# Performance work log

Measured on AMD Instinct MI355X. Metric: run time of the kernel, lower is better.

Reference implementation:

```python
import jax, jax.numpy as jnp
import numpy as np

B, S, H = 2, 1024, 2048          # batch, seq, hidden_size
I = 7168                          # intermediate_size
E = 8                             # num_local_experts
TOPK = 2                          # num_experts_per_tok
R = int(I * H * 0.1 / (I + H))    # delta_low_rank = 159


def setup_inputs() -> dict:
    key = jax.random.key(0)
    ks = jax.random.split(key, 12)
    s = 0.02
    return {
        "hidden_states": jax.random.normal(ks[0], (B, S, H), jnp.float32),
        "gate_w": jax.random.normal(ks[1], (E, H), jnp.float32) * s,
        "W1": jax.random.normal(ks[2], (E, I, H), jnp.float32) * s,
        "W2": jax.random.normal(ks[3], (E, H, I), jnp.float32) * s,
        "W3": jax.random.normal(ks[4], (E, I, H), jnp.float32) * s,
        "U1": jax.random.normal(ks[5], (E, I, R), jnp.float32) * s,
        "V1": jax.random.normal(ks[6], (E, R, H), jnp.float32) * s,
        "U2": jax.random.normal(ks[7], (E, H, R), jnp.float32) * s,
        "V2": jax.random.normal(ks[8], (E, R, I), jnp.float32) * s,
        "U3": jax.random.normal(ks[9], (E, I, R), jnp.float32) * s,
        "V3": jax.random.normal(ks[10], (E, R, H), jnp.float32) * s,
    }


def reference(hidden_states, gate_w, W1, W2, W3, U1, V1, U2, V2, U3, V3):
    b, s, h = hidden_states.shape
    x = hidden_states.reshape(-1, h)                     # [T, H]
    T = x.shape[0]
    router_logits = x @ gate_w.T                          # [T, E]
    probs = jax.nn.softmax(router_logits.astype(jnp.float32), axis=-1)
    rw, sel = jax.lax.top_k(probs, TOPK)                  # [T, k]
    rw = rw / jnp.sum(rw, axis=-1, keepdims=True)
    rw = rw.astype(x.dtype)
    # dense combine weights: zero for unselected experts (same math as gather/scatter)
    comb = jnp.zeros((T, E), x.dtype).at[jnp.arange(T)[:, None], sel].add(rw)
    out = jnp.zeros_like(x)
    for e in range(E):                                    # small fixed expert loop
        up = x @ W3[e].T + (x @ V3[e].T) @ U3[e].T        # [T, I]
        gate = x @ W1[e].T + (x @ V1[e].T) @ U1[e].T      # [T, I]
        hmid = jax.nn.silu(gate) * up                     # [T, I]
        y = hmid @ W2[e].T + (hmid @ V2[e].T) @ U2[e].T   # [T, H]
        out = out + comb[:, e, None] * y
    return out.reshape(b, s, h), router_logits
```

## Files before the change

kernel.cpp:

```cpp
#include <hip/hip_runtime.h>
#include <cstdint>
#include <cstddef>

#define TT 2048
#define HH 2048
#define II 7168
#define EE 8
#define RR 159
#define RPAD 192
#define ROWS 4096

typedef __attribute__((ext_vector_type(8))) short bf16x8;
typedef __attribute__((ext_vector_type(4))) float f32x4;

__device__ __forceinline__ unsigned short f2bf(float f) {
  unsigned int u = __float_as_uint(f);
  u += 0x7fffu + ((u >> 16) & 1u);
  return (unsigned short)(u >> 16);
}
__device__ __forceinline__ bf16x8 zero8() {
  bf16x8 v;
#pragma unroll
  for (int j = 0; j < 8; j++) v[j] = 0;
  return v;
}
__device__ __forceinline__ void gload16(const unsigned short* g, unsigned short* l) {
  __builtin_amdgcn_global_load_lds(
      (const __attribute__((address_space(1))) unsigned int*)g,
      (__attribute__((address_space(3))) unsigned int*)l, 16, 0, 0);
}

__global__ __launch_bounds__(256) void k_f2bf_flat(const float* __restrict__ s,
                                                   unsigned short* __restrict__ d,
                                                   long long n8) {
  long long i = (long long)blockIdx.x * blockDim.x + threadIdx.x;
  long long stride = (long long)gridDim.x * blockDim.x;
  for (; i < n8; i += stride) {
    const float* p = s + i * 8;
    float4 a = *(const float4*)p;
    float4 b = *(const float4*)(p + 4);
    bf16x8 v;
    v[0] = (short)f2bf(a.x); v[1] = (short)f2bf(a.y);
    v[2] = (short)f2bf(a.z); v[3] = (short)f2bf(a.w);
    v[4] = (short)f2bf(b.x); v[5] = (short)f2bf(b.y);
    v[6] = (short)f2bf(b.z); v[7] = (short)f2bf(b.w);
    *(bf16x8*)(d + i * 8) = v;
  }
}

__global__ __launch_bounds__(256) void k_upad(const float* __restrict__ U,
                                              unsigned short* __restrict__ Up, int rows) {
  long long idx = (long long)blockIdx.x * 256 + threadIdx.x;
  long long total = (long long)rows * 24;
  if (idx >= total) return;
  int row = (int)(idx / 24), c8 = (int)(idx % 24);
  unsigned short* dp = Up + (size_t)row * RPAD + c8 * 8;
#pragma unroll
  for (int j = 0; j < 8; j++) {
    int c = c8 * 8 + j;
    dp[j] = (c < RR) ? f2bf(U[(size_t)row * RR + c]) : (unsigned short)0;
  }
}

__global__ __launch_bounds__(256) void k_router(
    const float* __restrict__ x, const float* __restrict__ gw,
    float* __restrict__ logits_out, int* __restrict__ sel,
    float* __restrict__ wtok, int* __restrict__ counts) {
  int t = blockIdx.x;
  const float* xr = x + (size_t)t * HH;
  int base = threadIdx.x * 8;
  float4 x0 = *(const float4*)(xr + base);
  float4 x1 = *(const float4*)(xr + base + 4);
  float part[EE];
#pragma unroll
  for (int e = 0; e < EE; e++) {
    const float* g = gw + (size_t)e * HH + base;
    float4 g0 = *(const float4*)g;
    float4 g1 = *(const float4*)(g + 4);
    part[e] = x0.x * g0.x + x0.y * g0.y + x0.z * g0.z + x0.w * g0.w +
              x1.x * g1.x + x1.y * g1.y + x1.z * g1.z + x1.w * g1.w;
  }
#pragma unroll
  for (int off = 32; off > 0; off >>= 1)
#pragma unroll
    for (int e = 0; e < EE; e++) part[e] += __shfl_down(part[e], off);
  __shared__ float red[4][EE];
  int w = threadIdx.x >> 6, lane = threadIdx.x & 63;
  if (lane == 0) {
#pragma unroll
    for (int e = 0; e < EE; e++) red[w][e] = part[e];
  }
  __syncthreads();
  if (threadIdx.x == 0) {
    float lg[EE];
    float mx = -1e30f;
#pragma unroll
    for (int e = 0; e < EE; e++) {
      lg[e] = red[0][e] + red[1][e] + red[2][e] + red[3][e];
      logits_out[(size_t)t * EE + e] = lg[e];
      mx = fmaxf(mx, lg[e]);
    }
// ... 79 lines not shown
  float* Pout = Pp + (size_t)blockIdx.z * ROWS * RPAD;
  int kt0 = split * kc;
  int kt1 = kt0 + kc;
  if (kt1 > K) kt1 = K;
  __shared__ unsigned short As[64 * 64];
  __shared__ unsigned short Bs[192 * 64];
  int tid = threadIdx.x, lane = tid & 63, w = tid >> 6;
  int rstage = tid >> 3, cg = tid & 7;
  f32x4 acc[12];
#pragma unroll
  for (int n = 0; n < 12; n++) acc[n] = (f32x4){0.f, 0.f, 0.f, 0.f};
  for (int kt = kt0; kt < kt1; kt += 64) {
#pragma unroll
    for (int p = 0; p < 2; p++) {
      int r = p * 32 + rstage;
      bf16x8 v = zero8();
      int gr = m0 + r;
      if (gr < cnt) {
        size_t arow = GATHER ? (size_t)rowsA[roff + gr] : (size_t)(roff + gr);
        v = *(const bf16x8*)(Ab + arow * (size_t)lda + kt + cg * 8);
      }
      *(bf16x8*)&As[r * 64 + ((cg ^ (r & 7)) * 8)] = v;
    }
#pragma unroll
    for (int p = 0; p < 6; p++) {
      int r = p * 32 + rstage;
      bf16x8 v = zero8();
      if (r < RR) v = *(const bf16x8*)(V + (size_t)r * K + kt + cg * 8);
      *(bf16x8*)&Bs[r * 64 + ((cg ^ (r & 7)) * 8)] = v;
    }
    __syncthreads();
#pragma unroll
    for (int ks = 0; ks < 2; ks++) {
      int rA = w * 16 + (lane & 15);
      bf16x8 a = *(const bf16x8*)&As[rA * 64 + (((ks * 4 + (lane >> 4)) ^ (rA & 7)) * 8)];
#pragma unroll
      for (int n = 0; n < 12; n++) {
        int rB = n * 16 + (lane & 15);
        bf16x8 b = *(const bf16x8*)&Bs[rB * 64 + (((ks * 4 + (lane >> 4)) ^ (rB & 7)) * 8)];
        acc[n] = __builtin_amdgcn_mfma_f32_16x16x32_bf16(a, b, acc[n], 0, 0, 0);
      }
    }
    __syncthreads();
  }
  int mbase = m0 + w * 16 + (lane >> 4) * 4;
#pragma unroll
  for (int n = 0; n < 12; n++) {
    int col = n * 16 + (lane & 15);
#pragma unroll
    for (int r4 = 0; r4 < 4; r4++) {
      int row = mbase + r4;
      if (row < cnt) Pout[(size_t)(roff + row) * RPAD + col] = acc[n][r4];
    }
  }
}

__global__ __launch_bounds__(256) void k_lr_reduce(
    const float* __restrict__ Pp, unsigned short* __restrict__ P0,
    unsigned short* __restrict__ P1m, int NS, int nmat) {
  long long idx = (long long)blockIdx.x * 256 + threadIdx.x;
  long long total = (long long)nmat * ROWS * 24;
  if (idx >= total) return;
  int mat = (int)(idx / ((long long)ROWS * 24));
  int rem = (int)(idx % ((long long)ROWS * 24));
  int row = rem / 24, c8 = rem % 24;
  const float* base = Pp + ((size_t)mat * NS) * ROWS * RPAD + (size_t)row * RPAD + c8 * 8;
  float s0 = 0, s1 = 0, s2 = 0, s3 = 0, s4 = 0, s5 = 0, s6 = 0, s7 = 0;
  for (int sp = 0; sp < NS; sp++) {
    const float* p = base + (size_t)sp * ROWS * RPAD;
    float4 a = *(const float4*)p;
    float4 b = *(const float4*)(p + 4);
    s0 += a.x; s1 += a.y; s2 += a.z; s3 += a.w;
    s4 += b.x; s5 += b.y; s6 += b.z; s7 += b.w;
  }
  bf16x8 v;
  v[0] = (short)f2bf(s0); v[1] = (short)f2bf(s1);
  v[2] = (short)f2bf(s2); v[3] = (short)f2bf(s3);
  v[4] = (short)f2bf(s4); v[5] = (short)f2bf(s5);
  v[6] = (short)f2bf(s6); v[7] = (short)f2bf(s7);
  unsigned short* P = (mat == 0) ? P0 : P1m;
  *(bf16x8*)(P + (size_t)row * RPAD + c8 * 8) = v;
}

template <bool GATHER>
__global__ __launch_bounds__(256, 2) void k_lowrank(
    const unsigned short* __restrict__ Ab, int lda, int K,
    const float* __restrict__ Vaf, const float* __restrict__ Vbf,
    unsigned short* __restrict__ Pa, unsigned short* __restrict__ Pb,
    const int* __restrict__ counts, const int* __restrict__ offs,
    const int* __restrict__ rowsA) {
  int e = blockIdx.y;
  int cnt = counts[e];
  int m0 = blockIdx.x * 64;
  if (m0 >= cnt) return;
  int roff = offs[e];
  unsigned short* P = (blockIdx.z == 0) ? Pa : Pb;
  __shared__ unsigned short As[64 * 64];
  __shared__ unsigned short Bs[192 * 64];
  int tid = threadIdx.x, lane = tid & 63, w = tid >> 6;
  int rstage = tid >> 3, cg = tid & 7;
  f32x4 acc[12];
#pragma unroll
  for (int n = 0; n < 12; n++) acc[n] = (f32x4){0.f, 0.f, 0.f, 0.f};
  for (int kt = 0; kt < K; kt += 64) {
#pragma unroll
    for (int p = 0; p < 2; p++) {
      int r = p * 32 + rstage;
      bf16x8 v = zero8();
      int gr = m0 + r;
      if (gr < cnt) {
        size_t arow = GATHER ? (size_t)rowsA[roff + gr] : (size_t)(roff + gr);
        v = *(const bf16x8*)(Ab + arow * (size_t)lda + kt + cg * 8);
      }
      *(bf16x8*)&As[r * 64 + ((cg ^ (r & 7)) * 8)] = v;
    }
#pragma unroll
    for (int p = 0; p < 6; p++) {
      int r = p * 32 + rstage;
      bf16x8 v = zero8();
      if (r < RR) {
        const float* V = ((blockIdx.z == 0) ? Vaf : Vbf) + (size_t)e * RR * K;
        const float* s = V + (size_t)r * K + kt + cg * 8;
        float4 a = *(const float4*)s;
        float4 b = *(const float4*)(s + 4);
        v[0] = (short)f2bf(a.x); v[1] = (short)f2bf(a.y);
        v[2] = (short)f2bf(a.z); v[3] = (short)f2bf(a.w);
        v[4] = (short)f2bf(b.x); v[5] = (short)f2bf(b.y);
        v[6] = (short)f2bf(b.z); v[7] = (short)f2bf(b.w);
      }
      *(bf16x8*)&Bs[r * 64 + ((cg ^ (r & 7)) * 8)] = v;
    }
    __syncthreads();
#pragma unroll
    for (int ks = 0; ks < 2; ks++) {
      int rA = w * 16 + (lane & 15);
      bf16x8 a = *(const bf16x8*)&As[rA * 64 + (((ks * 4 + (lane >> 4)) ^ (rA & 7)) * 8)];
#pragma unroll
      for (int n = 0; n < 12; n++) {
        int rB = n * 16 + (lane & 15);
        bf16x8 b = *(const bf16x8*)&Bs[rB * 64 + (((ks * 4 + (lane >> 4)) ^ (rB & 7)) * 8)];
        acc[n] = __builtin_amdgcn_mfma_f32_16x16x32_bf16(a, b, acc[n], 0, 0, 0);
      }
    }
    __syncthreads();
  }
  int mbase = m0 + w * 16 + (lane >> 4) * 4;
#pragma unroll
  for (int n = 0; n < 12; n++) {
    int col = n * 16 + (lane & 15);
#pragma unroll
    for (int r4 = 0; r4 < 4; r4++) {
      int row = mbase + r4;
      if (row < cnt) P[(size_t)(roff + row) * RPAD + col] = f2bf(acc[n][r4]);
    }
  }
}

template <bool PRE>
__global__ __launch_bounds__(256, 2) void k_mlp1(
    const unsigned short* __restrict__ Xb,
    const float* __restrict__ W1f, const float* __restrict__ W3f,
    const unsigned short* __restrict__ W1b, const unsigned short* __restrict__ W3b,
    const unsigned short* __restrict__ P1, const unsigned short* __restrict__ P3,
    const float* __restrict__ U1f, const float* __restrict__ U3f,
    const unsigned short* __restrict__ U1p, const unsigned short* __restrict__ U3p,
    unsigned short* __restrict__ hmid,
    const int* __restrict__ counts, const int* __restrict__ offs,
    const int* __restrict__ rowsA) {
  int e = blockIdx.z;
  int cnt = counts[e];
  int m0 = blockIdx.y * 128;
  if (m0 >= cnt) return;
  int n0 = blockIdx.x * 128;
  int roff = offs[e];
  __shared__ unsigned short As[128 * 64];
  __shared__ unsigned short Bg[128 * 64];
  __shared__ unsigned short Bu[128 * 64];
  int tid = threadIdx.x, lane = tid & 63, w = tid >> 6;
  int wr = (w >> 1) * 64, wc = (w & 1) * 64;
  int rstage = tid >> 3, cg = tid & 7;
  f32x4 accg[4][4], accu[4][4];
#pragma unroll
  for (int m = 0; m < 4; m++)
#pragma unroll
    for (int n = 0; n < 4; n++) {
      accg[m][n] = (f32x4){0.f, 0.f, 0.f, 0.f};
      accu[m][n] = (f32x4){0.f, 0.f, 0.f, 0.f};
    }
  int srow = (w << 5) + (lane >> 3);
  int swz = (((lane & 7) ^ ((lane >> 3) & 7)) << 3);
  const unsigned short* pa[4];
  const unsigned short* pg[4];
  const unsigned short* pu[4];
  if constexpr (PRE) {
    const unsigned short* w1 = W1b + (size_t)e * II * HH;
    const unsigned short* w3 = W3b + (size_t)e * II * HH;
#pragma unroll
    for (int i = 0; i < 4; i++) {
      int gr = m0 + srow + i * 8;
      if (gr >= cnt) gr = cnt - 1;
      pa[i] = Xb + (size_t)rowsA[roff + gr] * HH + swz;
      pg[i] = w1 + (size_t)(n0 + srow + i * 8) * HH + swz;
      pu[i] = w3 + (size_t)(n0 + srow + i * 8) * HH + swz;
    }
  }
  for (int kt = 0; kt < HH; kt += 64) {
    if constexpr (PRE) {
#pragma unroll
      for (int i = 0; i < 4; i++) {
        unsigned short* la = &As[(((w << 5) + (i << 3))) * 64];
        unsigned short* lg = &Bg[(((w << 5) + (i << 3))) * 64];
        unsigned short* lu = &Bu[(((w << 5) + (i << 3))) * 64];
        gload16(pa[i] + kt, la);
        gload16(pg[i] + kt, lg);
        gload16(pu[i] + kt, lu);
      }
    } else {
      const float* w1 = W1f + (size_t)e * II * HH;
      const float* w3 = W3f + (size_t)e * II * HH;
#pragma unroll
      for (int p = 0; p < 4; p++) {
        int r = p * 32 + rstage;
        bf16x8 v = zero8();
        int gr = m0 + r;
        if (gr < cnt) {
          size_t arow = (size_t)rowsA[roff + gr];
          v = *(const bf16x8*)(Xb + arow * HH + kt + cg * 8);
        }
        *(bf16x8*)&As[r * 64 + ((cg ^ (r & 7)) * 8)] = v;
      }
#pragma unroll
      for (int p = 0; p < 4; p++) {
        int r = p * 32 + rstage;
        size_t rowb = (size_t)(n0 + r);
        const float* s1 = w1 + rowb * HH + kt + cg * 8;
        const float* s3 = w3 + rowb * HH + kt + cg * 8;
        float4 a0 = *(const float4*)s1, a1 = *(const float4*)(s1 + 4);
        float4 b0 = *(const float4*)s3, b1 = *(const float4*)(s3 + 4);
        bf16x8 vg, vu;
        vg[0] = (short)f2bf(a0.x); vg[1] = (short)f2bf(a0.y);
        vg[2] = (short)f2bf(a0.z); vg[3] = (short)f2bf(a0.w);
        vg[4] = (short)f2bf(a1.x); vg[5] = (short)f2bf(a1.y);
        vg[6] = (short)f2bf(a1.z); vg[7] = (short)f2bf(a1.w);
        vu[0] = (short)f2bf(b0.x); vu[1] = (short)f2bf(b0.y);
        vu[2] = (short)f2bf(b0.z); vu[3] = (short)f2bf(b0.w);
        vu[4] = (short)f2bf(b1.x); vu[5] = (short)f2bf(b1.y);
        vu[6] = (short)f2bf(b1.z); vu[7] = (short)f2bf(b1.w);
        int idx = r * 64 + ((cg ^ (r & 7)) * 8);
        *(bf16x8*)&Bg[idx] = vg;
        *(bf16x8*)&Bu[idx] = vu;
      }
    }
    __syncthreads();
#pragma unroll
    for (int ks = 0; ks < 2; ks++) {
      bf16x8 af[4], bg[4], bu[4];
#pragma unroll
      for (int m = 0; m < 4; m++) {
        int r = wr + m * 16 + (lane & 15);
        af[m] = *(const bf16x8*)&As[r * 64 + (((ks * 4 + (lane >> 4)) ^ (r & 7)) * 8)];
      }
#pragma unroll
      for (int n = 0; n < 4; n++) {
        int r = wc + n * 16 + (lane & 15);
        int idx = r * 64 + (((ks * 4 + (lane >> 4)) ^ (r & 7)) * 8);
        bg[n] = *(const bf16x8*)&Bg[idx];
        bu[n] = *(const bf16x8*)&Bu[idx];
      }
#pragma unroll
      for (int m = 0; m < 4; m++)
#pragma unroll
        for (int n = 0; n < 4; n++) {
          accg[m][n] = __builtin_amdgcn_mfma_f32_16x16x32_bf16(af[m], bg[n], accg[m][n], 0, 0, 0);
          accu[m][n] = __builtin_amdgcn_mfma_f32_16x16x32_bf16(af[m], bu[n], accu[m][n], 0, 0, 0);
        }
    }
    __syncthreads();
  }
  for (int kt = 0; kt < RPAD; kt += 64) {
    if constexpr (PRE) {
      const unsigned short* u1 = U1p + (size_t)e * II * RPAD;
#pragma unroll
      for (int i = 0; i < 4; i++) {
        int gr = m0 + srow + i * 8;
        if (gr >= cnt) gr = cnt - 1;
        gload16(P1 + (size_t)(roff + gr) * RPAD + swz + kt,
                &As[(((w << 5) + (i << 3))) * 64]);
        gload16(u1 + (size_t)(n0 + srow + i * 8) * RPAD + swz + kt,
                &Bg[(((w << 5) + (i << 3))) * 64]);
      }
    } else {
      const float* u1 = U1f + (size_t)e * II * RR;
#pragma unroll
      for (int p = 0; p < 4; p++) {
        int r = p * 32 + rstage;
        bf16x8 v = zero8();
        int gr = m0 + r;
        if (gr < cnt) v = *(const bf16x8*)(P1 + (size_t)(roff + gr) * RPAD + kt + cg * 8);
        *(bf16x8*)&As[r * 64 + ((cg ^ (r & 7)) * 8)] = v;
      }
#pragma unroll
      for (int p = 0; p < 4; p++) {
        int r = p * 32 + rstage;
        const float* s = u1 + (size_t)(n0 + r) * RR;
        bf16x8 v;
#pragma unroll
        for (int j = 0; j < 8; j++) {
          int k = kt + cg * 8 + j;
          v[j] = (short)(k < RR ? f2bf(s[k]) : (unsigned short)0);
        }
        *(bf16x8*)&Bg[r * 64 + ((cg ^ (r & 7)) * 8)] = v;
      }
    }
    __syncthreads();
#pragma unroll
    for (int ks = 0; ks < 2; ks++) {
      bf16x8 af[4], bg[4];
#pragma unroll
      for (int m = 0; m < 4; m++) {
        int r = wr + m * 16 + (lane & 15);
        af[m] = *(const bf16x8*)&As[r * 64 + (((ks * 4 + (lane >> 4)) ^ (r & 7)) * 8)];
      }
#pragma unroll
      for (int n = 0; n < 4; n++) {
        int r = wc + n * 16 + (lane & 15);
        bg[n] = *(const bf16x8*)&Bg[r * 64 + (((ks * 4 + (lane >> 4)) ^ (r & 7)) * 8)];
      }
#pragma unroll
      for (int m = 0; m < 4; m++)
#pragma unroll
        for (int n = 0; n < 4; n++)
          accg[m][n] = __builtin_amdgcn_mfma_f32_16x16x32_bf16(af[m], bg[n], accg[m][n], 0, 0, 0);
    }
    __syncthreads();
    if constexpr (PRE) {
      const unsigned short* u3 = U3p + (size_t)e * II * RPAD;
#pragma unroll
      for (int i = 0; i < 4; i++) {
        int gr = m0 + srow + i * 8;
        if (gr >= cnt) gr = cnt - 1;
        gload16(P3 + (size_t)(roff + gr) * RPAD + swz + kt,
                &As[(((w << 5) + (i << 3))) * 64]);
        gload16(u3 + (size_t)(n0 + srow + i * 8) * RPAD + swz + kt,
                &Bu[(((w << 5) + (i << 3))) * 64]);
      }
    } else {
      const float* u3 = U3f + (size_t)e * II * RR;
#pragma unroll
      for (int p = 0; p < 4; p++) {
        int r = p * 32 + rstage;
        bf16x8 v = zero8();
        int gr = m0 + r;
        if (gr < cnt) v = *(const bf16x8*)(P3 + (size_t)(roff + gr) * RPAD + kt + cg * 8);
        *(bf16x8*)&As[r * 64 + ((cg ^ (r & 7)) * 8)] = v;
      }
#pragma unroll
      for (int p = 0; p < 4; p++) {
        int r = p * 32 + rstage;
        const float* s = u3 + (size_t)(n0 + r) * RR;
        bf16x8 v;
#pragma unroll
        for (int j = 0; j < 8; j++) {
          int k = kt + cg * 8 + j;
          v[j] = (short)(k < RR ? f2bf(s[k]) : (unsigned short)0);
        }
        *(bf16x8*)&Bu[r * 64 + ((cg ^ (r & 7)) * 8)] = v;
      }
    }
    __syncthreads();
#pragma unroll
    for (int ks = 0; ks < 2; ks++) {
      bf16x8 af[4], bu[4];
#pragma unroll
      for (int m = 0; m < 4; m++) {
        int r = wr + m * 16 + (lane & 15);
        af[m] = *(const bf16x8*)&As[r * 64 + (((ks * 4 + (lane >> 4)) ^ (r & 7)) * 8)];
      }
#pragma unroll
      for (int n = 0; n < 4; n++) {
        int r = wc + n * 16 + (lane & 15);
        bu[n] = *(const bf16x8*)&Bu[r * 64 + (((ks * 4 + (lane >> 4)) ^ (r & 7)) * 8)];
      }
#pragma unroll
      for (int m = 0; m < 4; m++)
#pragma unroll
        for (int n = 0; n < 4; n++)
          accu[m][n] = __builtin_amdgcn_mfma_f32_16x16x32_bf16(af[m], bu[n], accu[m][n], 0, 0, 0);
    }
    __syncthreads();
  }
#pragma unroll
  for (int m = 0; m < 4; m++) {
#pragma unroll
    for (int r4 = 0; r4 < 4; r4++) {
      int row = m0 + wr + m * 16 + (lane >> 4) * 4 + r4;
      if (row < cnt) {
        size_t rb = (size_t)(roff + row) * II + n0 + wc;
#pragma unroll
        for (int n = 0; n < 4; n++) {
          float g = accg[m][n][r4], uu = accu[m][n][r4];
          float h = (g / (1.f + __expf(-g))) * uu;
          hmid[rb + n * 16 + (lane & 15)] = f2bf(h);
        }
      }
    }
  }
}

template <bool PRE>
__global__ __launch_bounds__(256, 2) void k_mlp2(
    const unsigned short* __restrict__ hmid,
    const float* __restrict__ W2f, const unsigned short* __restrict__ W2b,
    const unsigned short* __restrict__ P2,
    const float* __restrict__ U2f, const unsigned short* __restrict__ U2p,
    const float* __restrict__ rowwgt, float* __restrict__ ybuf,
    const int* __restrict__ counts, const int* __restrict__ offs) {
  int e = blockIdx.z;
  int cnt = counts[e];
  int m0 = blockIdx.y * 128;
  if (m0 >= cnt) return;
  int n0 = blockIdx.x * 128;
  int roff = offs[e];
  __shared__ unsigned short As[128 * 64];
  __shared__ unsigned short Bs[128 * 64];
  int tid = threadIdx.x, lane = tid & 63, w = tid >> 6;
  int wr = (w >> 1) * 64, wc = (w & 1) * 64;
  int rstage = tid >> 3, cg = tid & 7;
  f32x4 acc[4][4];
#pragma unroll
  for (int m = 0; m < 4; m++)
#pragma unroll
    for (int n = 0; n < 4; n++) acc[m][n] = (f32x4){0.f, 0.f, 0.f, 0.f};
  int srow = (w << 5) + (lane >> 3);
  int swz = (((lane & 7) ^ ((lane >> 3) & 7)) << 3);
  const unsigned short* pa[4];
  const unsigned short* pb[4];
  if constexpr (PRE) {
    const unsigned short* w2 = W2b + (size_t)e * HH * II;
#pragma unroll
    for (int i = 0; i < 4; i++) {
      int gr = m0 + srow + i * 8;
      if (gr >= cnt) gr = cnt - 1;
      pa[i] = hmid + (size_t)(roff + gr) * II + swz;
      pb[i] = w2 + (size_t)(n0 + srow + i * 8) * II + swz;
    }
  }
  for (int kt = 0; kt < II; kt += 64) {
    if constexpr (PRE) {
#pragma unroll
      for (int i = 0; i < 4; i++) {
        gload16(pa[i] + kt, &As[(((w << 5) + (i << 3))) * 64]);
        gload16(pb[i] + kt, &Bs[(((w << 5) + (i << 3))) * 64]);
      }
    } else {
      const float* w2 = W2f + (size_t)e * HH * II;
#pragma unroll
      for (int p = 0; p < 4; p++) {
        int r = p * 32 + rstage;
        bf16x8 v = zero8();
        int gr = m0 + r;
        if (gr < cnt) v = *(const bf16x8*)(hmid + (size_t)(roff + gr) * II + kt + cg * 8);
        *(bf16x8*)&As[r * 64 + ((cg ^ (r & 7)) * 8)] = v;
      }
#pragma unroll
      for (int p = 0; p < 4; p++) {
        int r = p * 32 + rstage;
        const float* s = w2 + (size_t)(n0 + r) * II + kt + cg * 8;
        float4 a = *(const float4*)s;
        float4 b = *(const float4*)(s + 4);
        bf16x8 v;
        v[0] = (short)f2bf(a.x); v[1] = (short)f2bf(a.y);
        v[2] = (short)f2bf(a.z); v[3] = (short)f2bf(a.w);
        v[4] = (short)f2bf(b.x); v[5] = (short)f2bf(b.y);
        v[6] = (short)f2bf(b.z); v[7] = (short)f2bf(b.w);
        *(bf16x8*)&Bs[r * 64 + ((cg ^ (r & 7)) * 8)] = v;
      }
    }
    __syncthreads();
#pragma unroll
    for (int ks = 0; ks < 2; ks++) {
      bf16x8 af[4], bs[4];
#pragma unroll
      for (int m = 0; m < 4; m++) {
        int r = wr + m * 16 + (lane & 15);
        af[m] = *(const bf16x8*)&As[r * 64 + (((ks * 4 + (lane >> 4)) ^ (r & 7)) * 8)];
      }
#pragma unroll
      for (int n = 0; n < 4; n++) {
        int r = wc + n * 16 + (lane & 15);
        bs[n] = *(const bf16x8*)&Bs[r * 64 + (((ks * 4 + (lane >> 4)) ^ (r & 7)) * 8)];
      }
#pragma unroll
      for (int m = 0; m < 4; m++)
#pragma unroll
        for (int n = 0; n < 4; n++)
          acc[m][n] = __builtin_amdgcn_mfma_f32_16x16x32_bf16(af[m], bs[n], acc[m][n], 0, 0, 0);
    }
    __syncthreads();
  }
  for (int kt = 0; kt < RPAD; kt += 64) {
    if constexpr (PRE) {
      const unsigned short* u2 = U2p + (size_t)e * HH * RPAD;
#pragma unroll
      for (int i = 0; i < 4; i++) {
        int gr = m0 + srow + i * 8;
        if (gr >= cnt) gr = cnt - 1;
        gload16(P2 + (size_t)(roff + gr) * RPAD + swz + kt,
                &As[(((w << 5) + (i << 3))) * 64]);
        gload16(u2 + (size_t)(n0 + srow + i * 8) * RPAD + swz + kt,
                &Bs[(((w << 5) + (i << 3))) * 64]);
      }
    } else {
      const float* u2 = U2f + (size_t)e * HH * RR;
#pragma unroll
      for (int p = 0; p < 4; p++) {
        int r = p * 32 + rstage;
        bf16x8 v = zero8();
        int gr = m0 + r;
        if (gr < cnt) v = *(const bf16x8*)(P2 + (size_t)(roff + gr) * RPAD + kt + cg * 8);
        *(bf16x8*)&As[r * 64 + ((cg ^ (r & 7)) * 8)] = v;
      }
#pragma unroll
      for (int p = 0; p < 4; p++) {
        int r = p * 32 + rstage;
        const float* s = u2 + (size_t)(n0 + r) * RR;
        bf16x8 v;
#pragma unroll
        for (int j = 0; j < 8; j++) {
          int k = kt + cg * 8 + j;
          v[j] = (short)(k < RR ? f2bf(s[k]) : (unsigned short)0);
        }
        *(bf16x8*)&Bs[r * 64 + ((cg ^ (r & 7)) * 8)] = v;
      }
    }
    __syncthreads();
#pragma unroll
    for (int ks = 0; ks < 2; ks++) {
      bf16x8 af[4], bs[4];
#pragma unroll
      for (int m = 0; m < 4; m++) {
        int r = wr + m * 16 + (lane & 15);
        af[m] = *(const bf16x8*)&As[r * 64 + (((ks * 4 + (lane >> 4)) ^ (r & 7)) * 8)];
      }
#pragma unroll
      for (int n = 0; n < 4; n++) {
        int r = wc + n * 16 + (lane & 15);
        bs[n] = *(const bf16x8*)&Bs[r * 64 + (((ks * 4 + (lane >> 4)) ^ (r & 7)) * 8)];
      }
#pragma unroll
      for (int m = 0; m < 4; m++)
#pragma unroll
        for (int n = 0; n < 4; n++)
          acc[m][n] = __builtin_amdgcn_mfma_f32_16x16x32_bf16(af[m], bs[n], acc[m][n], 0, 0, 0);
    }
    __syncthreads();
  }
#pragma unroll
  for (int m = 0; m < 4; m++) {
#pragma unroll
    for (int r4 = 0; r4 < 4; r4++) {
      int row = m0 + wr + m * 16 + (lane >> 4) * 4 + r4;
      if (row < cnt) {
        float wgt = rowwgt[roff + row];
        size_t rb = (size_t)(roff + row) * HH + n0 + wc;
#pragma unroll
        for (int n = 0; n < 4; n++)
          ybuf[rb + n * 16 + (lane & 15)] = acc[m][n][r4] * wgt;
      }
    }
  }
}

__global__ void k_combine(const float* __restrict__ ybuf, const int* __restrict__ rowid,
                          float* __restrict__ out) {
  int idx = blockIdx.x * 256 + threadIdx.x;
  int t = idx >> 8;
  int c = (idx & 255) * 8;
  int r0 = rowid[t * 2], r1 = rowid[t * 2 + 1];
  const float* y0 = ybuf + (size_t)r0 * HH + c;
  const float* y1 = ybuf + (size_t)r1 * HH + c;
  float4 a0 = *(const float4*)y0, a1 = *(const float4*)(y0 + 4);
  float4 b0 = *(const float4*)y1, b1 = *(const float4*)(y1 + 4);
  float4 o0 = {a0.x + b0.x, a0.y + b0.y, a0.z + b0.z, a0.w + b0.w};
  float4 o1 = {a1.x + b1.x, a1.y + b1.y, a1.z + b1.z, a1.w + b1.w};
  float* o = out + (size_t)t * HH + c;
  *(float4*)o = o0;
  *(float4*)(o + 4) = o1;
}

extern "C" void kernel_launch(void* const* d_in, const int* in_sizes, int n_in,
                              void* d_out, int out_size, void* d_ws, size_t ws_size,
                              hipStream_t stream) {
  const float* x  = (const float*)d_in[0];
  const float* gw = (const float*)d_in[1];
  const float* W1 = (const float*)d_in[2];
  const float* W2 = (const float*)d_in[3];
  const float* W3 = (const float*)d_in[4];
  const float* U1 = (const float*)d_in[5];
  const float* V1 = (const float*)d_in[6];
  const float* U2 = (const float*)d_in[7];
  const float* V2 = (const float*)d_in[8];
  const float* U3 = (const float*)d_in[9];
  const float* V3 = (const float*)d_in[10];
  float* out = (float*)d_out;
  float* logits = out + (size_t)TT * HH;

  char* ws = (char*)d_ws;
  size_t off = 0;
  auto take = [&](size_t b) -> char* {
    char* p = ws + off;
    off += (b + 255) & ~(size_t)255;
    return p;
  };
  unsigned short* Xb   = (unsigned short*)take((size_t)TT * HH * 2);
  unsigned short* hmid = (unsigned short*)take((size_t)ROWS * II * 2);
  unsigned short* P1   = (unsigned short*)take((size_t)ROWS * RPAD * 2);
  unsigned short* P3   = (unsigned short*)take((size_t)ROWS * RPAD * 2);
  unsigned short* P2   = (unsigned short*)take((size_t)ROWS * RPAD * 2);
  float* ybuf          = (float*)take((size_t)ROWS * HH * 4);
  int* sel             = (int*)take((size_t)TT * 2 * 4);
  float* wtok          = (float*)take((size_t)TT * 2 * 4);
  int* rowsA           = (int*)take((size_t)ROWS * 4);
  float* rowwgt        = (float*)take((size_t)ROWS * 4);
  int* rowid           = (int*)take((size_t)TT * 2 * 4);
  int* meta            = (int*)take(1024);
  int* counts  = meta;
  int* offs    = meta + 16;
  int* curs    = meta + 32;
  unsigned short* W1b = (unsigned short*)take((size_t)EE * II * HH * 2);
  unsigned short* W3b = (unsigned short*)take((size_t)EE * II * HH * 2);
  unsigned short* W2b = (unsigned short*)take((size_t)EE * HH * II * 2);
  unsigned short* V1b = (unsigned short*)take((size_t)EE * RR * HH * 2);
  unsigned short* V3b = (unsigned short*)take((size_t)EE * RR * HH * 2);
  unsigned short* V2b = (unsigned short*)take((size_t)EE * RR * II * 2);
  unsigned short* U1p = (unsigned short*)take((size_t)EE * II * RPAD * 2);
  unsigned short* U3p = (unsigned short*)take((size_t)EE * II * RPAD * 2);
  unsigned short* U2p = (unsigned short*)take((size_t)EE * HH * RPAD * 2);
  float* Pp           = (float*)take((size_t)8 * ROWS * RPAD * 4);
  size_t need = off;
  bool pre = (ws_size >= need);

  hipMemsetAsync(counts, 0, EE * sizeof(int), stream);
  if (pre) {
    k_f2bf_flat<<<4096, 256, 0, stream>>>(W1, W1b, (long long)EE * II * HH / 8);
    k_f2bf_flat<<<4096, 256, 0, stream>>>(W3, W3b, (long long)EE * II * HH / 8);
    k_f2bf_flat<<<4096, 256, 0, stream>>>(W2, W2b, (long long)EE * HH * II / 8);
    k_f2bf_flat<<<1024, 256, 0, stream>>>(V1, V1b, (long long)EE * RR * HH / 8);
    k_f2bf_flat<<<1024, 256, 0, stream>>>(V3, V3b, (long long)EE * RR * HH / 8);
    k_f2bf_flat<<<1024, 256, 0, stream>>>(V2, V2b, (long long)EE * RR * II / 8);
    k_upad<<<(EE * II * 24 + 255) / 256, 256, 0, stream>>>(U1, U1p, EE * II);
    k_upad<<<(EE * II * 24 + 255) / 256, 256, 0, stream>>>(U3, U3p, EE * II);
    k_upad<<<(EE * HH * 24 + 255) / 256, 256, 0, stream>>>(U2, U2p, EE * HH);
  }
  k_router<<<TT, 256, 0, stream>>>(x, gw, logits, sel, wtok, counts);
  k_offsets<<<1, 64, 0, stream>>>(counts, offs, curs);
  k_build<<<TT / 256, 256, 0, stream>>>(sel, wtok, curs, rowsA, rowwgt, rowid);
  k_x2bf<<<2048, 256, 0, stream>>>(x, Xb);
  if (pre) {
    k_lowrank_sk<true><<<dim3(TT / 64, EE, 2 * 4), 256, 0, stream>>>(
        Xb, HH, HH, 512, 4, V1b, V3b, Pp, counts, offs, rowsA);
    k_lr_reduce<<<(2 * ROWS * 24 + 255) / 256, 256, 0, stream>>>(Pp, P1, P3, 4, 2);
    k_mlp1<true><<<dim3(II / 128, TT / 128, EE), 256, 0, stream>>>(
        Xb, W1, W3, W1b, W3b, P1, P3, U1, U3, U1p, U3p, hmid, counts, offs, rowsA);
    k_lowrank_sk<false><<<dim3(TT / 64, EE, 8), 256, 0, stream>>>(
        hmid, II, II, 896, 8, V2b, V2b, Pp, counts, offs, rowsA);
    k_lr_reduce<<<(ROWS * 24 + 255) / 256, 256, 0, stream>>>(Pp, P2, P2, 8, 1);
    k_mlp2<true><<<dim3(HH / 128, TT / 128, EE), 256, 0, stream>>>(
        hmid, W2, W2b, P2, U2, U2p, rowwgt, ybuf, counts, offs);
  } else {
    k_lowrank<true><<<dim3(TT / 64, EE, 2), 256, 0, stream>>>(
        Xb, HH, HH, V1, V3, P1, P3, counts, offs, rowsA);
    k_mlp1<false><<<dim3(II / 128, TT / 128, EE), 256, 0, stream>>>(
        Xb, W1, W3, W1b, W3b, P1, P3, U1, U3, U1p, U3p, hmid, counts, offs, rowsA);
    k_lowrank<false><<<dim3(TT / 64, EE, 1), 256, 0, stream>>>(
        hmid, II, II, V2, V2, P2, P2, counts, offs, rowsA);
    k_mlp2<false><<<dim3(HH / 128, TT / 128, EE), 256, 0, stream>>>(
        hmid, W2, W2b, P2, U2, U2p, rowwgt, ybuf, counts, offs);
  }
  k_combine<<<(TT * HH / 8) / 256, 256, 0, stream>>>(ybuf, rowid, out);
}
```

Baseline: 1.311 ms.

## Convert large expert weights to bf16 inside GEMMs with register prefetch

Drops the separate passes that converted W1, W3 and W2 to bf16 in a workspace. The GEMM kernels now read fp32 weights directly, prefetch the next k-tile into registers, and pack them to bf16 with v_cvt_pk_bf16_f32 before storing to LDS. This removes a large write-and-reread of bf16 weight copies. The cost is that each weight tile is fetched as fp32, twice the bytes, and read again by every m-tile block. The low-rank U1/U3 loop is also restructured so the P3 and U3 loads share LDS buffers.

```diff
diff --git a/kernel.cpp b/kernel.cpp
--- a/kernel.cpp
+++ b/kernel.cpp
@@ -17,6 +17,11 @@
   unsigned int u = __float_as_uint(f);
   u += 0x7fffu + ((u >> 16) & 1u);
   return (unsigned short)(u >> 16);
+}
+__device__ __forceinline__ unsigned int cvtpk(float lo, float hi) {
+  unsigned int r;
+  asm volatile("v_cvt_pk_bf16_f32 %0, %1, %2" : "=v"(r) : "v"(lo), "v"(hi));
+  return r;
 }
 __device__ __forceinline__ bf16x8 zero8() {
   bf16x8 v;
@@ -262,87 +267,10 @@
   *(bf16x8*)(P + (size_t)row * RPAD + c8 * 8) = v;
 }
 
-template <bool GATHER>
-__global__ __launch_bounds__(256, 2) void k_lowrank(
-    const unsigned short* __restrict__ Ab, int lda, int K,
-    const float* __restrict__ Vaf, const float* __restrict__ Vbf,
-    unsigned short* __restrict__ Pa, unsigned short* __restrict__ Pb,
-    const int* __restrict__ counts, const int* __restrict__ offs,
-    const int* __restrict__ rowsA) {
-  int e = blockIdx.y;
-  int cnt = counts[e];
-  int m0 = blockIdx.x * 64;
-  if (m0 >= cnt) return;
-  int roff = offs[e];
-  unsigned short* P = (blockIdx.z == 0) ? Pa : Pb;
-  __shared__ unsigned short As[64 * 64];
-  __shared__ unsigned short Bs[192 * 64];
-  int tid = threadIdx.x, lane = tid & 63, w = tid >> 6;
-  int rstage = tid >> 3, cg = tid & 7;
-  f32x4 acc[12];
-#pragma unroll
-  for (int n = 0; n < 12; n++) acc[n] = (f32x4){0.f, 0.f, 0.f, 0.f};
-  for (int kt = 0; kt < K; kt += 64) {
-#pragma unroll
-    for (int p = 0; p < 2; p++) {
-      int r = p * 32 + rstage;
-      bf16x8 v = zero8();
-      int gr = m0 + r;
-      if (gr < cnt) {
-        size_t arow = GATHER ? (size_t)rowsA[roff + gr] : (size_t)(roff + gr);
-        v = *(const bf16x8*)(Ab + arow * (size_t)lda + kt + cg * 8);
-      }
-      *(bf16x8*)&As[r * 64 + ((cg ^ (r & 7)) * 8)] = v;
-    }
-#pragma unroll
-    for (int p = 0; p < 6; p++) {
-      int r = p * 32 + rstage;
-      bf16x8 v = zero8();
-      if (r < RR) {
-        const float* V = ((blockIdx.z == 0) ? Vaf : Vbf) + (size_t)e * RR * K;
-        const float* s = V + (size_t)r * K + kt + cg * 8;
-        float4 a = *(const float4*)s;
-        float4 b = *(const float4*)(s + 4);
-        v[0] = (short)f2bf(a.x); v[1] = (short)f2bf(a.y);
-        v[2] = (short)f2bf(a.z); v[3] = (short)f2bf(a.w);
-        v[4] = (short)f2bf(b.x); v[5] = (short)f2bf(b.y);
-        v[6] = (short)f2bf(b.z); v[7] = (short)f2bf(b.w);
-      }
-      *(bf16x8*)&Bs[r * 64 + ((cg ^ (r & 7)) * 8)] = v;
-    }
-    __syncthreads();
-#pragma unroll
-    for (int ks = 0; ks < 2; ks++) {
-      int rA = w * 16 + (lane & 15);
-      bf16x8 a = *(const bf16x8*)&As[rA * 64 + (((ks * 4 + (lane >> 4)) ^ (rA & 7)) * 8)];
-#pragma unroll
-      for (int n = 0; n < 12; n++) {
-        int rB = n * 16 + (lane & 15);
-        bf16x8 b = *(const bf16x8*)&Bs[rB * 64 + (((ks * 4 + (lane >> 4)) ^ (rB & 7)) * 8)];
-        acc[n] = __builtin_amdgcn_mfma_f32_16x16x32_bf16(a, b, acc[n], 0, 0, 0);
-      }
-    }
-    __syncthreads();
-  }
-  int mbase = m0 + w * 16 + (lane >> 4) * 4;
-#pragma unroll
-  for (int n = 0; n < 12; n++) {
-    int col = n * 16 + (lane & 15);
-#pragma unroll
-    for (int r4 = 0; r4 < 4; r4++) {
-      int row = mbase + r4;
-      if (row < cnt) P[(size_t)(roff + row) * RPAD + col] = f2bf(acc[n][r4]);
-    }
-  }
-}
-
-template <bool PRE>
 __global__ __launch_bounds__(256, 2) void k_mlp1(
     const unsigned short* __restrict__ Xb,
     const float* __restrict__ W1f, const float* __restrict__ W3f,
-    const unsigned short* __restrict__ W1b, const unsigned short* __restrict__ W3b,
     const unsigned short* __restrict__ P1, const unsigned short* __restrict__ P3,
-    const float* __restrict__ U1f, const float* __restrict__ U3f,
     const unsigned short* __restrict__ U1p, const unsigned short* __restrict__ U3p,
     unsigned short* __restrict__ hmid,
     const int* __restrict__ counts, const int* __restrict__ offs,
@@ -358,7 +286,6 @@
   __shared__ unsigned short Bu[128 * 64];
   int tid = threadIdx.x, lane = tid & 63, w = tid >> 6;
   int wr = (w >> 1) * 64, wc = (w & 1) * 64;
-  int rstage = tid >> 3, cg = tid & 7;
   f32x4 accg[4][4], accu[4][4];
 #pragma unroll
   for (int m = 0; m < 4; m++)
@@ -369,69 +296,58 @@
     }
   int srow = (w << 5) + (lane >> 3);
   int swz = (((lane & 7) ^ ((lane >> 3) & 7)) << 3);
+  int lrow0 = (w << 5) + (lane >> 3);
+  int lidx = 0;
   const unsigned short* pa[4];
-  const unsigned short* pg[4];
-  const unsigned short* pu[4];
-  if constexpr (PRE) {
-    const unsigned short* w1 = W1b + (size_t)e * II * HH;
-    const unsigned short* w3 = W3b + (size_t)e * II * HH;
+  const float* pw1[4];
+  const float* pw3[4];
+  {
+    const float* w1 = W1f + (size_t)e * II * HH;
+    const float* w3 = W3f + (size_t)e * II * HH;
 #pragma unroll
     for (int i = 0; i < 4; i++) {
       int gr = m0 + srow + i * 8;
       if (gr >= cnt) gr = cnt - 1;
       pa[i] = Xb + (size_t)rowsA[roff + gr] * HH + swz;
-      pg[i] = w1 + (size_t)(n0 + srow + i * 8) * HH + swz;
-      pu[i] = w3 + (size_t)(n0 + srow + i * 8) * HH + swz;
-    }
+      pw1[i] = w1 + (size_t)(n0 + srow + i * 8) * HH + swz;
+      pw3[i] = w3 + (size_t)(n0 + srow + i * 8) * HH + swz;
+    }
+  }
+  float4 rg[4][2], ru[4][2];
+#pragma unroll
+  for (int i = 0; i < 4; i++) {
+    rg[i][0] = *(const float4*)(pw1[i]);
+    rg[i][1] = *(const float4*)(pw1[i] + 4);
+    ru[i][0] = *(const float4*)(pw3[i]);
+    ru[i][1] = *(const float4*)(pw3[i] + 4);
   }
   for (int kt = 0; kt < HH; kt += 64) {
-    if constexpr (PRE) {
+#pragma unroll
+    for (int i = 0; i < 4; i++) {
+      gload16(pa[i] + kt, &As[(((w << 5) + (i << 3))) * 64]);
+      int idx = (lrow0 + i * 8) * 64 + (lane & 7) * 8;
+      uint4 qg, qu;
+      qg.x = cvtpk(rg[i][0].x, rg[i][0].y);
+      qg.y = cvtpk(rg[i][0].z, rg[i][0].w);
+      qg.z = cvtpk(rg[i][1].x, rg[i][1].y);
+      qg.w = cvtpk(rg[i][1].z, rg[i][1].w);
+      qu.x = cvtpk(ru[i][0].x, ru[i][0].y);
+      qu.y = cvtpk(ru[i][0].z, ru[i][0].w);
+      qu.z = cvtpk(ru[i][1].x, ru[i][1].y);
+      qu.w = cvtpk(ru[i][1].z, ru[i][1].w);
+      *(uint4*)&Bg[idx] = qg;
+      *(uint4*)&Bu[idx] = qu;
+    }
+    __syncthreads();
+    if (kt + 64 < HH) {
 #pragma unroll
       for (int i = 0; i < 4; i++) {
-        unsigned short* la = &As[(((w << 5) + (i << 3))) * 64];
-        unsigned short* lg = &Bg[(((w << 5) + (i << 3))) * 64];
-        unsigned short* lu = &Bu[(((w << 5) + (i << 3))) * 64];
-        gload16(pa[i] + kt, la);
-        gload16(pg[i] + kt, lg);
-        gload16(pu[i] + kt, lu);
-      }
-    } else {
-      const float* w1 = W1f + (size_t)e * II * HH;
-      const float* w3 = W3f + (size_t)e * II * HH;
-#pragma unroll
-      for (int p = 0; p < 4; p++) {
-        int r = p * 32 + rstage;
-        bf16x8 v = zero8();
-        int gr = m0 + r;
-        if (gr < cnt) {
-          size_t arow = (size_t)rowsA[roff + gr];
-          v = *(const bf16x8*)(Xb + arow * HH + kt + cg * 8);
-        }
-        *(bf16x8*)&As[r * 64 + ((cg ^ (r & 7)) * 8)] = v;
-      }
-#pragma unroll
-      for (int p = 0; p < 4; p++) {
-        int r = p * 32 + rstage;
-        size_t rowb = (size_t)(n0 + r);
-        const float* s1 = w1 + rowb * HH + kt + cg * 8;
-        const float* s3 = w3 + rowb * HH + kt + cg * 8;
-        float4 a0 = *(const float4*)s1, a1 = *(const float4*)(s1 + 4);
-        float4 b0 = *(const float4*)s3, b1 = *(const float4*)(s3 + 4);
-        bf16x8 vg, vu;
-        vg[0] = (short)f2bf(a0.x); vg[1] = (short)f2bf(a0.y);
-        vg[2] = (short)f2bf(a0.z); vg[3] = (short)f2bf(a0.w);
-        vg[4] = (short)f2bf(a1.x); vg[5] = (short)f2bf(a1.y);
-        vg[6] = (short)f2bf(a1.z); vg[7] = (short)f2bf(a1.w);
-        vu[0] = (short)f2bf(b0.x); vu[1] = (short)f2bf(b0.y);
-        vu[2] = (short)f2bf(b0.z); vu[3] = (short)f2bf(b0.w);
-        vu[4] = (short)f2bf(b1.x); vu[5] = (short)f2bf(b1.y);
-        vu[6] = (short)f2bf(b1.z); vu[7] = (short)f2bf(b1.w);
-        int idx = r * 64 + ((cg ^ (r & 7)) * 8);
-        *(bf16x8*)&Bg[idx] = vg;
-        *(bf16x8*)&Bu[idx] = vu;
-      }
-    }
-    __syncthreads();
+        rg[i][0] = *(const float4*)(pw1[i] + kt + 64);
+        rg[i][1] = *(const float4*)(pw1[i] + kt + 68);
+        ru[i][0] = *(const float4*)(pw3[i] + kt + 64);
+        ru[i][1] = *(const float4*)(pw3[i] + kt + 68);
+      }
+    }
 #pragma unroll
     for (int ks = 0; ks < 2; ks++) {
       bf16x8 af[4], bg[4], bu[4];
@@ -458,39 +374,18 @@
     __syncthreads();
   }
   for (int kt = 0; kt < RPAD; kt += 64) {
-    if constexpr (PRE) {
-      const unsigned short* u1 = U1p + (size_t)e * II * RPAD;
-#pragma unroll
-      for (int i = 0; i < 4; i++) {
-        int gr = m0 + srow + i * 8;
-        if (gr >= cnt) gr = cnt - 1;
-        gload16(P1 + (size_t)(roff + gr) * RPAD + swz + kt,
-                &As[(((w << 5) + (i << 3))) * 64]);
-        gload16(u1 + (size_t)(n0 + srow + i * 8) * RPAD + swz + kt,
-                &Bg[(((w << 5) + (i << 3))) * 64]);
-      }
-    } else {
-      const float* u1 = U1f + (size_t)e * II * RR;
-#pragma unroll
-      for (int p = 0; p < 4; p++) {
-        int r = p * 32 + rstage;
-        bf16x8 v = zero8();
-        int gr = m0 + r;
-        if (gr < cnt) v = *(const bf16x8*)(P1 + (size_t)(roff + gr) * RPAD + kt + cg * 8);
-        *(bf16x8*)&As[r * 64 + ((cg ^ (r & 7)) * 8)] = v;
-      }
-#pragma unroll
-      for (int p = 0; p < 4; p++) {
-        int r = p * 32 + rstage;
-        const float* s = u1 + (size_t)(n0 + r) * RR;
-        bf16x8 v;
-#pragma unroll
-        for (int j = 0; j < 8; j++) {
-          int k = kt + cg * 8 + j;
-          v[j] = (short)(k < RR ? f2bf(s[k]) : (unsigned short)0);
-        }
-        *(bf16x8*)&Bg[r * 64 + ((cg ^ (r & 7)) * 8)] = v;
-      }
+    const unsigned short* u1 = U1p + (size_t)e * II * RPAD;
+    const unsigned short* u3 = U3p + (size_t)e * II * RPAD;
+#pragma unroll
+    for (int i = 0; i < 4; i++) {
+      int gr = m0 + srow + i * 8;
+      if (gr >= cnt) gr = cnt - 1;
+      gload16(P1 + (size_t)(roff + gr) * RPAD + swz + kt,
+              &As[(((w << 5) + (i << 3))) * 64]);
+      gload16(u1 + (size_t)(n0 + srow + i * 8) * RPAD + swz + kt,
+              &Bg[(((w << 5) + (i << 3))) * 64]);
+      gload16(P3 + (size_t)(roff + gr) * RPAD + swz + kt,
+              &Bu[(((w << 5) + (i << 3))) * 64]);
     }
     __syncthreads();
 #pragma unroll
@@ -513,39 +408,10 @@
           accg[m][n] = __builtin_amdgcn_mfma_f32_16x16x32_bf16(af[m], bg[n], accg[m][n], 0, 0, 0);
     }
     __syncthreads();
-    if constexpr (PRE) {
-      const unsigned short* u3 = U3p + (size_t)e * II * RPAD;
-#pragma unroll
-      for (int i = 0; i < 4; i++) {
-        int gr = m0 + srow + i * 8;
-        if (gr >= cnt) gr = cnt - 1;
-        gload16(P3 + (size_t)(roff + gr) * RPAD + swz + kt,
-                &As[(((w << 5) + (i << 3))) * 64]);
-        gload16(u3 + (size_t)(n0 + srow + i * 8) * RPAD + swz + kt,
-                &Bu[(((w << 5) + (i << 3))) * 64]);
-      }
-    } else {
-      const float* u3 = U3f + (size_t)e * II * RR;
-#pragma unroll
-      for (int p = 0; p < 4; p++) {
-        int r = p * 32 + rstage;
-        bf16x8 v = zero8();
-        int gr = m0 + r;
-        if (gr < cnt) v = *(const bf16x8*)(P3 + (size_t)(roff + gr) * RPAD + kt + cg * 8);
-        *(bf16x8*)&As[r * 64 + ((cg ^ (r & 7)) * 8)] = v;
-      }
-#pragma unroll
-      for (int p = 0; p < 4; p++) {
-        int r = p * 32 + rstage;
-        const float* s = u3 + (size_t)(n0 + r) * RR;
-        bf16x8 v;
-#pragma unroll
-        for (int j = 0; j < 8; j++) {
-          int k = kt + cg * 8 + j;
-          v[j] = (short)(k < RR ? f2bf(s[k]) : (unsigned short)0);
-        }
-        *(bf16x8*)&Bu[r * 64 + ((cg ^ (r & 7)) * 8)] = v;
-      }
+#pragma unroll
+    for (int i = 0; i < 4; i++) {
+      gload16(u3 + (size_t)(n0 + srow + i * 8) * RPAD + swz + kt,
+              &Bg[(((w << 5) + (i << 3))) * 64]);
     }
     __syncthreads();
 #pragma unroll
@@ -554,12 +420,12 @@
 #pragma unroll
       for (int m = 0; m < 4; m++) {
         int r = wr + m * 16 + (lane & 15);
-        af[m] = *(const bf16x8*)&As[r * 64 + (((ks * 4 + (lane >> 4)) ^ (r & 7)) * 8)];
+        af[m] = *(const bf16x8*)&Bu[r * 64 + (((ks * 4 + (lane >> 4)) ^ (r & 7)) * 8)];
       }
 #pragma unroll
       for (int n = 0; n < 4; n++) {
         int r = wc + n * 16 + (lane & 15);
-        bu[n] = *(const bf16x8*)&Bu[r * 64 + (((ks * 4 + (lane >> 4)) ^ (r & 7)) * 8)];
+        bu[n] = *(const bf16x8*)&Bg[r * 64 + (((ks * 4 + (lane >> 4)) ^ (r & 7)) * 8)];
       }
 #pragma unroll
       for (int m = 0; m < 4; m++)
@@ -587,12 +453,11 @@
   }
 }
 
-template <bool PRE>
 __global__ __launch_bounds__(256, 2) void k_mlp2(
     const unsigned short* __restrict__ hmid,
-    const float* __restrict__ W2f, const unsigned short* __restrict__ W2b,
+    const float* __restrict__ W2f,
     const unsigned short* __restrict__ P2,
-    const float* __restrict__ U2f, const unsigned short* __restrict__ U2p,
+    const unsigned short* __restrict__ U2p,
     const float* __restrict__ rowwgt, float* __restrict__ ybuf,
     const int* __restrict__ counts, const int* __restrict__ offs) {
   int e = blockIdx.z;
@@ -605,7 +470,6 @@
   __shared__ unsigned short Bs[128 * 64];
   int tid = threadIdx.x, lane = tid & 63, w = tid >> 6;
   int wr = (w >> 1) * 64, wc = (w & 1) * 64;
-  int rstage = tid >> 3, cg = tid & 7;
   f32x4 acc[4][4];
 #pragma unroll
   for (int m = 0; m < 4; m++)
@@ -613,50 +477,45 @@
     for (int n = 0; n < 4; n++) acc[m][n] = (f32x4){0.f, 0.f, 0.f, 0.f};
   int srow = (w << 5) + (lane >> 3);
   int swz = (((lane & 7) ^ ((lane >> 3) & 7)) << 3);
+  int lrow0 = (w << 5) + (lane >> 3);
   const unsigned short* pa[4];
-  const unsigned short* pb[4];
-  if constexpr (PRE) {
-    const unsigned short* w2 = W2b + (size_t)e * HH * II;
+  const float* pw2[4];
+  {
+    const float* w2 = W2f + (size_t)e * HH * II;
 #pragma unroll
     for (int i = 0; i < 4; i++) {
       int gr = m0 + srow + i * 8;
       if (gr >= cnt) gr = cnt - 1;
       pa[i] = hmid + (size_t)(roff + gr) * II + swz;
-      pb[i] = w2 + (size_t)(n0 + srow + i * 8) * II + swz;
-    }
+      pw2[i] = w2 + (size_t)(n0 + srow + i * 8) * II + swz;
+    }
+  }
+  float4 rb[4][2];
+#pragma unroll
+  for (int i = 0; i < 4; i++) {
+    rb[i][0] = *(const float4*)(pw2[i]);
+    rb[i][1] = *(const float4*)(pw2[i] + 4);
   }
   for (int kt = 0; kt < II; kt += 64) {
-    if constexpr (PRE) {
+#pragma unroll
+    for (int i = 0; i < 4; i++) {
+      gload16(pa[i] + kt, &As[(((w << 5) + (i << 3))) * 64]);
+      int idx = (lrow0 + i * 8) * 64 + (lane & 7) * 8;
+      uint4 q;
+      q.x = cvtpk(rb[i][0].x, rb[i][0].y);
+      q.y = cvtpk(rb[i][0].z, rb[i][0].w);
+      q.z = cvtpk(rb[i][1].x, rb[i][1].y);
+      q.w = cvtpk(rb[i][1].z, rb[i][1].w);
+      *(uint4*)&Bs[idx] = q;
+    }
+    __syncthreads();
+    if (kt + 64 < II) {
 #pragma unroll
       for (int i = 0; i < 4; i++) {
-        gload16(pa[i] + kt, &As[(((w << 5) + (i << 3))) * 64]);
-        gload16(pb[i] + kt, &Bs[(((w << 5) + (i << 3))) * 64]);
-      }
-    } else {
-      const float* w2 = W2f + (size_t)e * HH * II;
-#pragma unroll
-      for (int p = 0; p < 4; p++) {
-        int r = p * 32 + rstage;
-        bf16x8 v = zero8();
-        int gr = m0 + r;
-        if (gr < cnt) v = *(const bf16x8*)(hmid + (size_t)(roff + gr) * II + kt + cg * 8);
-        *(bf16x8*)&As[r * 64 + ((cg ^ (r & 7)) * 8)] = v;
-      }
-#pragma unroll
-      for (int p = 0; p < 4; p++) {
-        int r = p * 32 + rstage;
-        const float* s = w2 + (size_t)(n0 + r) * II + kt + cg * 8;
-        float4 a = *(const float4*)s;
-        float4 b = *(const float4*)(s + 4);
-        bf16x8 v;
-        v[0] = (short)f2bf(a.x); v[1] = (short)f2bf(a.y);
-        v[2] = (short)f2bf(a.z); v[3] = (short)f2bf(a.w);
-        v[4] = (short)f2bf(b.x); v[5] = (short)f2bf(b.y);
-        v[6] = (short)f2bf(b.z); v[7] = (short)f2bf(b.w);
-        *(bf16x8*)&Bs[r * 64 + ((cg ^ (r & 7)) * 8)] = v;
-      }
-    }
-    __syncthreads();
+        rb[i][0] = *(const float4*)(pw2[i] + kt + 64);
+        rb[i][1] = *(const float4*)(pw2[i] + kt + 68);
+      }
+    }
 #pragma unroll
     for (int ks = 0; ks < 2; ks++) {
       bf16x8 af[4], bs[4];
@@ -679,39 +538,15 @@
     __syncthreads();
   }
   for (int kt = 0; kt < RPAD; kt += 64) {
-    if constexpr (PRE) {
-      const unsigned short* u2 = U2p + (size_t)e * HH * RPAD;
-#pragma unroll
-      for (int i = 0; i < 4; i++) {
-        int gr = m0 + srow + i * 8;
-        if (gr >= cnt) gr = cnt - 1;
-        gload16(P2 + (size_t)(roff + gr) * RPAD + swz + kt,
-                &As[(((w << 5) + (i << 3))) * 64]);
-        gload16(u2 + (size_t)(n0 + srow + i * 8) * RPAD + swz + kt,
-                &Bs[(((w << 5) + (i << 3))) * 64]);
-      }
-    } else {
-      const float* u2 = U2f + (size_t)e * HH * RR;
-#pragma unroll
-      for (int p = 0; p < 4; p++) {
-        int r = p * 32 + rstage;
-        bf16x8 v = zero8();
-        int gr = m0 + r;
-        if (gr < cnt) v = *(const bf16x8*)(P2 + (size_t)(roff + gr) * RPAD + kt + cg * 8);
-        *(bf16x8*)&As[r * 64 + ((cg ^ (r & 7)) * 8)] = v;
-      }
-#pragma unroll
-      for (int p = 0; p < 4; p++) {
-        int r = p * 32 + rstage;
-        const float* s = u2 + (size_t)(n0 + r) * RR;
-        bf16x8 v;
-#pragma unroll
-        for (int j = 0; j < 8; j++) {
-          int k = kt + cg * 8 + j;
-          v[j] = (short)(k < RR ? f2bf(s[k]) : (unsigned short)0);
-        }
-        *(bf16x8*)&Bs[r * 64 + ((cg ^ (r & 7)) * 8)] = v;
-      }
+    const unsigned short* u2 = U2p + (size_t)e * HH * RPAD;
+#pragma unroll
+    for (int i = 0; i < 4; i++) {
+      int gr = m0 + srow + i * 8;
+      if (gr >= cnt) gr = cnt - 1;
+      gload16(P2 + (size_t)(roff + gr) * RPAD + swz + kt,
+              &As[(((w << 5) + (i << 3))) * 64]);
+      gload16(u2 + (size_t)(n0 + srow + i * 8) * RPAD + swz + kt,
+              &Bs[(((w << 5) + (i << 3))) * 64]);
     }
     __syncthreads();
 #pragma unroll
@@ -742,10 +577,10 @@
       int row = m0 + wr + m * 16 + (lane >> 4) * 4 + r4;
       if (row < cnt) {
         float wgt = rowwgt[roff + row];
-        size_t rb = (size_t)(roff + row) * HH + n0 + wc;
+        size_t rb2 = (size_t)(roff + row) * HH + n0 + wc;
 #pragma unroll
         for (int n = 0; n < 4; n++)
-          ybuf[rb + n * 16 + (lane & 15)] = acc[m][n][r4] * wgt;
+          ybuf[rb2 + n * 16 + (lane & 15)] = acc[m][n][r4] * wgt;
       }
     }
   }
@@ -807,9 +642,6 @@
   int* counts  = meta;
   int* offs    = meta + 16;
   int* curs    = meta + 32;
-  unsigned short* W1b = (unsigned short*)take((size_t)EE * II * HH * 2);
-  unsigned short* W3b = (unsigned short*)take((size_t)EE * II * HH * 2);
-  unsigned short* W2b = (unsigned short*)take((size_t)EE * HH * II * 2);
   unsigned short* V1b = (unsigned short*)take((size_t)EE * RR * HH * 2);
   unsigned short* V3b = (unsigned short*)take((size_t)EE * RR * HH * 2);
   unsigned short* V2b = (unsigned short*)take((size_t)EE * RR * II * 2);
@@ -817,45 +649,27 @@
   unsigned short* U3p = (unsigned short*)take((size_t)EE * II * RPAD * 2);
   unsigned short* U2p = (unsigned short*)take((size_t)EE * HH * RPAD * 2);
   float* Pp           = (float*)take((size_t)8 * ROWS * RPAD * 4);
-  size_t need = off;
-  bool pre = (ws_size >= need);
 
   hipMemsetAsync(counts, 0, EE * sizeof(int), stream);
-  if (pre) {
-    k_f2bf_flat<<<4096, 256, 0, stream>>>(W1, W1b, (long long)EE * II * HH / 8);
-    k_f2bf_flat<<<4096, 256, 0, stream>>>(W3, W3b, (long long)EE * II * HH / 8);
-    k_f2bf_flat<<<4096, 256, 0, stream>>>(W2, W2b, (long long)EE * HH * II / 8);
-    k_f2bf_flat<<<1024, 256, 0, stream>>>(V1, V1b, (long long)EE * RR * HH / 8);
-    k_f2bf_flat<<<1024, 256, 0, stream>>>(V3, V3b, (long long)EE * RR * HH / 8);
-    k_f2bf_flat<<<1024, 256, 0, stream>>>(V2, V2b, (long long)EE * RR * II / 8);
-    k_upad<<<(EE * II * 24 + 255) / 256, 256, 0, stream>>>(U1, U1p, EE * II);
-    k_upad<<<(EE * II * 24 + 255) / 256, 256, 0, stream>>>(U3, U3p, EE * II);
-    k_upad<<<(EE * HH * 24 + 255) / 256, 256, 0, stream>>>(U2, U2p, EE * HH);
-  }
+  k_f2bf_flat<<<1024, 256, 0, stream>>>(V1, V1b, (long long)EE * RR * HH / 8);
+  k_f2bf_flat<<<1024, 256, 0, stream>>>(V3, V3b, (long long)EE * RR * HH / 8);
+  k_f2bf_flat<<<1024, 256, 0, stream>>>(V2, V2b, (long long)EE * RR * II / 8);
+  k_upad<<<(EE * II * 24 + 255) / 256, 256, 0, stream>>>(U1, U1p, EE * II);
+  k_upad<<<(EE * II * 24 + 255) / 256, 256, 0, stream>>>(U3, U3p, EE * II);
+  k_upad<<<(EE * HH * 24 + 255) / 256, 256, 0, stream>>>(U2, U2p, EE * HH);
   k_router<<<TT, 256, 0, stream>>>(x, gw, logits, sel, wtok, counts);
   k_offsets<<<1, 64, 0, stream>>>(counts, offs, curs);
   k_build<<<TT / 256, 256, 0, stream>>>(sel, wtok, curs, rowsA, rowwgt, rowid);
   k_x2bf<<<2048, 256, 0, stream>>>(x, Xb);
-  if (pre) {
-    k_lowrank_sk<true><<<dim3(TT / 64, EE, 2 * 4), 256, 0, stream>>>(
-        Xb, HH, HH, 512, 4, V1b, V3b, Pp, counts, offs, rowsA);
-    k_lr_reduce<<<(2 * ROWS * 24 + 255) / 256, 256, 0, stream>>>(Pp, P1, P3, 4, 2);
-    k_mlp1<true><<<dim3(II / 128, TT / 128, EE), 256, 0, stream>>>(
-        Xb, W1, W3, W1b, W3b, P1, P3, U1, U3, U1p, U3p, hmid, counts, offs, rowsA);
-    k_lowrank_sk<false><<<dim3(TT / 64, EE, 8), 256, 0, stream>>>(
-        hmid, II, II, 896, 8, V2b, V2b, Pp, counts, offs, rowsA);
-    k_lr_reduce<<<(ROWS * 24 + 255) / 256, 256, 0, stream>>>(Pp, P2, P2, 8, 1);
-    k_mlp2<true><<<dim3(HH / 128, TT / 128, EE), 256, 0, stream>>>(
-        hmid, W2, W2b, P2, U2, U2p, rowwgt, ybuf, counts, offs);
-  } else {
-    k_lowrank<true><<<dim3(TT / 64, EE, 2), 256, 0, stream>>>(
-        Xb, HH, HH, V1, V3, P1, P3, counts, offs, rowsA);
-    k_mlp1<false><<<dim3(II / 128, TT / 128, EE), 256, 0, stream>>>(
-        Xb, W1, W3, W1b, W3b, P1, P3, U1, U3, U1p, U3p, hmid, counts, offs, rowsA);
-    k_lowrank<false><<<dim3(TT / 64, EE, 1), 256, 0, stream>>>(
-        hmid, II, II, V2, V2, P2, P2, counts, offs, rowsA);
-    k_mlp2<false><<<dim3(HH / 128, TT / 128, EE), 256, 0, stream>>>(
-        hmid, W2, W2b, P2, U2, U2p, rowwgt, ybuf, counts, offs);
-  }
+  k_lowrank_sk<true><<<dim3(TT / 64, EE, 2 * 4), 256, 0, stream>>>(
+      Xb, HH, HH, 512, 4, V1b, V3b, Pp, counts, offs, rowsA);
+  k_lr_reduce<<<(2 * ROWS * 24 + 255) / 256, 256, 0, stream>>>(Pp, P1, P3, 4, 2);
+  k_mlp1<<<dim3(II / 128, TT / 128, EE), 256, 0, stream>>>(
+      Xb, W1, W3, P1, P3, U1p, U3p, hmid, counts, offs, rowsA);
+  k_lowrank_sk<false><<<dim3(TT / 64, EE, 8), 256, 0, stream>>>(
+      hmid, II, II, 896, 8, V2b, V2b, Pp, counts, offs, rowsA);
+  k_lr_reduce<<<(ROWS * 24 + 255) / 256, 256, 0, stream>>>(Pp, P2, P2, 8, 1);
+  k_mlp2<<<dim3(HH / 128, TT / 128, EE), 256, 0, stream>>>(
+      hmid, W2, P2, U2p, rowwgt, ybuf, counts, offs);
   k_combine<<<(TT * HH / 8) / 256, 256, 0, stream>>>(ybuf, rowid, out);
 }
```

Result: slower. 1.762 ms (+34.3%).
